# Performance work log

Measured on AMD Instinct MI355X. Metric: run time of the kernel, lower is better.

## Reference

```python
import jax, jax.numpy as jnp
import numpy as np

H = 32  # hidden_size hardcoded in CHIVE
T, B = 2048, 2048
D_F, D_P, D_S = 8, 8, 24


def setup_inputs() -> dict:
    key = jax.random.key(0)
    ks = jax.random.split(key, 16)
    s = 0.1  # weight scale
    return {
        "frnn_seq": jax.random.normal(ks[0], (T, B, D_F), jnp.float32),
        "phrnn_seq": jax.random.normal(ks[1], (T, B, D_P), jnp.float32),
        "sylrnn_seq": jax.random.normal(ks[2], (T, B, D_S), jnp.float32),
        "Wx_f": jax.random.normal(ks[3], (D_F, H), jnp.float32) * s,
        "Wh_f": jax.random.normal(ks[4], (H, H), jnp.float32) * s,
        "b_f": jnp.zeros((H,), jnp.float32),
        "Wx_p": jax.random.normal(ks[5], (D_P, H), jnp.float32) * s,
        "Wh_p": jax.random.normal(ks[6], (H, H), jnp.float32) * s,
        "b_p": jnp.zeros((H,), jnp.float32),
        "Wx_s": jax.random.normal(ks[7], (H, H), jnp.float32) * s,
        "Wh_s": jax.random.normal(ks[8], (H, H), jnp.float32) * s,
        "b_s": jnp.zeros((H,), jnp.float32),
        "frnn_clock": jax.random.randint(ks[9], (T,), 0, 8, jnp.int32),
        "phrnn_clock": jax.random.randint(ks[10], (T,), 0, 8, jnp.int32),
        "sample_freq": jax.random.randint(ks[11], (T,), 0, 2, jnp.int32),
    }


def reference(frnn_seq, phrnn_seq, sylrnn_seq,
              Wx_f, Wh_f, b_f, Wx_p, Wh_p, b_p, Wx_s, Wh_s, b_s,
              frnn_clock, phrnn_clock, sample_freq):
    # Clockwork cell: update h only when timestep % clock_val == 0.
    # Clocks are offset +1 so the modulus is always >= 1.
    t_idx = jnp.arange(T)
    upd_f = (t_idx % (frnn_clock + 1)) == 0          # [T] bool
    upd_p = (t_idx % (phrnn_clock + 1)) == 0
    # the syl layer updates exactly when sample_freq[t] == 1.
    upd_s = sample_freq == 1

    # Static pad of syl input to max_length = max(H, H, D_S) = H (D_S <= H).
    syl_padded = jnp.pad(sylrnn_seq, ((0, 0), (0, 0), (0, H - D_S)))  # [T,B,H]

    def cell(x, h, Wx, Wh, b, upd):
        h_new = jnp.tanh(x @ Wx + h @ Wh + b)
        return jnp.where(upd, h_new, h)

    def step(carry, inputs):
        h_f, h_p, h_s = carry
        x_f, x_p, x_s, uf, up, us = inputs
        h_f = cell(x_f, h_f, Wx_f, Wh_f, b_f, uf)        # [B,H]
        h_p = cell(x_p, h_p, Wx_p, Wh_p, b_p, up)        # [B,H]
        x_stack = jnp.stack([h_f, h_p, x_s], axis=0)     # [3,B,H]
        h_s = cell(x_stack, h_s, Wx_s, Wh_s, b_s, us)    # [3,B,H]
        return (h_f, h_p, h_s), None

    h0 = jnp.zeros((B, H), frnn_seq.dtype)
    h0s = jnp.zeros((3, B, H), frnn_seq.dtype)
    (h_f, h_p, h_s), _ = jax.lax.scan(
        step, (h0, h0, h0s),
        (frnn_seq, phrnn_seq, syl_padded, upd_f, upd_p, upd_s))
    return h_s
```

## Files before the change

kernel.cpp:

```cpp
#include <hip/hip_runtime.h>


constexpr int TS  = 2048;
constexpr int B   = 2048;
constexpr int HH  = 32;
constexpr int CH  = 16;
constexpr int NCH = TS / CH;
constexpr int BPB = 8;

__device__ __forceinline__ float fast_tanh(float x) {
    x = fminf(fmaxf(x, -9.0f), 9.0f);
    float e = __expf(2.0f * x);
    return (e - 1.0f) * __builtin_amdgcn_rcpf(e + 1.0f);
}

__global__ __launch_bounds__(256, 1)
void chive_rnn(const float* __restrict__ frnn, const float* __restrict__ phrnn,
               const float* __restrict__ syl,
               const float* __restrict__ Wxf, const float* __restrict__ Whf,
               const float* __restrict__ bf,
               const float* __restrict__ Wxp, const float* __restrict__ Whp,
               const float* __restrict__ bp,
               const float* __restrict__ Wxs, const float* __restrict__ Whs,
               const float* __restrict__ bs,
               const int* __restrict__ fclock, const int* __restrict__ pclock,
               const int* __restrict__ sfreq, float* __restrict__ out)
{
    __shared__ __align__(16) float xfb[2][CH][BPB * 8];
    __shared__ __align__(16) float xpb[2][CH][BPB * 8];
    __shared__ __align__(16) float xsb[2][CH][BPB * 24];
    __shared__ __align__(16) float hf[BPB][HH];
    __shared__ __align__(16) float hp[BPB][HH];
    __shared__ __align__(16) float hs[3][BPB][HH];
    __shared__ int gates[TS];

    const int tid = threadIdx.x;
    const int j   = tid & 31;
    const int g   = tid >> 5;
    const int b0  = blockIdx.x * BPB;

    float wxf[8], whf_r[32], wxp[8], whp_r[32], wxs_r[32], whs_r[32];
#pragma unroll
    for (int i = 0; i < 8;  i++) wxf[i]   = Wxf[i * HH + j];
#pragma unroll
    for (int i = 0; i < 32; i++) whf_r[i] = Whf[i * HH + j];
#pragma unroll
    for (int i = 0; i < 8;  i++) wxp[i]   = Wxp[i * HH + j];
#pragma unroll
    for (int i = 0; i < 32; i++) whp_r[i] = Whp[i * HH + j];
#pragma unroll
    for (int i = 0; i < 32; i++) wxs_r[i] = Wxs[i * HH + j];
#pragma unroll
    for (int i = 0; i < 32; i++) whs_r[i] = Whs[i * HH + j];
    const float bfj = bf[j], bpj = bp[j], bsj = bs[j];

    float4 rf, rp, rs0, rs1, rs2;
    const int tl = tid >> 4;
    const int q  = tid & 15;

    auto load_chunk = [&](int ch) {
        const size_t t  = (size_t)ch * CH + tl;
        const float* fb = frnn  + (t * B + b0) * 8;
        const float* pb = phrnn + (t * B + b0) * 8;
        const float* sb = syl   + (t * B + b0) * 24;
        rf  = *(const float4*)(fb + q * 4);
        rp  = *(const float4*)(pb + q * 4);
        rs0 = *(const float4*)(sb + q * 4);
        rs1 = *(const float4*)(sb + 64 + q * 4);
        rs2 = *(const float4*)(sb + 128 + q * 4);
    };
    auto store_chunk = [&](int buf) {
        *(float4*)&xfb[buf][tl][q * 4]       = rf;
        *(float4*)&xpb[buf][tl][q * 4]       = rp;
        *(float4*)&xsb[buf][tl][q * 4]       = rs0;
        *(float4*)&xsb[buf][tl][64 + q * 4]  = rs1;
        *(float4*)&xsb[buf][tl][128 + q * 4] = rs2;
    };

    load_chunk(0);

    for (int i = tid; i < TS; i += 256) {
        int mf = fclock[i] + 1;
        int mp = pclock[i] + 1;
        int v = 0;
        if ((i % mf) == 0)  v |= 1;
        if ((i % mp) == 0)  v |= 2;
        if (sfreq[i] == 1)  v |= 4;
        gates[i] = v;
    }

    hf[g][j] = 0.f; hp[g][j] = 0.f;
    hs[0][g][j] = 0.f; hs[1][g][j] = 0.f; hs[2][g][j] = 0.f;

    store_chunk(0);
    __syncthreads();

    int cur = 0;
#pragma unroll 1
    for (int ch = 0; ch < NCH; ch++) {
        if (ch + 1 < NCH) load_chunk(ch + 1);

#pragma unroll 1
        for (int c = 0; c < CH; c++) {
            const int t  = ch * CH + c;
            const int gt = __builtin_amdgcn_readfirstlane(gates[t]);

            if (gt & 1) {
                float4 a = {bfj, 0.f, 0.f, 0.f};
                const float4* xv = (const float4*)&xfb[cur][c][g * 8];
                float4 x0 = xv[0], x1 = xv[1];
                a.x = fmaf(x0.x, wxf[0], a.x); a.y = fmaf(x0.y, wxf[1], a.y);
                a.z = fmaf(x0.z, wxf[2], a.z); a.w = fmaf(x0.w, wxf[3], a.w);
                a.x = fmaf(x1.x, wxf[4], a.x); a.y = fmaf(x1.y, wxf[5], a.y);
                a.z = fmaf(x1.z, wxf[6], a.z); a.w = fmaf(x1.w, wxf[7], a.w);
#pragma unroll
                for (int kk = 0; kk < 8; kk++) {
                    float4 h4 = *(const float4*)&hf[g][kk * 4];
                    a.x = fmaf(h4.x, whf_r[kk*4+0], a.x);
                    a.y = fmaf(h4.y, whf_r[kk*4+1], a.y);
                    a.z = fmaf(h4.z, whf_r[kk*4+2], a.z);
                    a.w = fmaf(h4.w, whf_r[kk*4+3], a.w);
                }
                hf[g][j] = fast_tanh((a.x + a.y) + (a.z + a.w));
            }

            if (gt & 2) {
                float4 a = {bpj, 0.f, 0.f, 0.f};
                const float4* xv = (const float4*)&xpb[cur][c][g * 8];
                float4 x0 = xv[0], x1 = xv[1];
                a.x = fmaf(x0.x, wxp[0], a.x); a.y = fmaf(x0.y, wxp[1], a.y);
                a.z = fmaf(x0.z, wxp[2], a.z); a.w = fmaf(x0.w, wxp[3], a.w);
                a.x = fmaf(x1.x, wxp[4], a.x); a.y = fmaf(x1.y, wxp[5], a.y);
                a.z = fmaf(x1.z, wxp[6], a.z); a.w = fmaf(x1.w, wxp[7], a.w);
#pragma unroll
                for (int kk = 0; kk < 8; kk++) {
                    float4 h4 = *(const float4*)&hp[g][kk * 4];
                    a.x = fmaf(h4.x, whp_r[kk*4+0], a.x);
                    a.y = fmaf(h4.y, whp_r[kk*4+1], a.y);
                    a.z = fmaf(h4.z, whp_r[kk*4+2], a.z);
                    a.w = fmaf(h4.w, whp_r[kk*4+3], a.w);
                }
                hp[g][j] = fast_tanh((a.x + a.y) + (a.z + a.w));
            }

            if (gt & 4) {
                float4 a0 = {bsj, 0.f, 0.f, 0.f};
                float4 a1 = {bsj, 0.f, 0.f, 0.f};
                float4 a2 = {bsj, 0.f, 0.f, 0.f};
#pragma unroll
                for (int kk = 0; kk < 8; kk++) {
                    float4 hf4 = *(const float4*)&hf[g][kk * 4];
                    float4 hp4 = *(const float4*)&hp[g][kk * 4];
                    float w0 = wxs_r[kk*4+0], w1 = wxs_r[kk*4+1];
                    float w2 = wxs_r[kk*4+2], w3 = wxs_r[kk*4+3];
                    a0.x = fmaf(hf4.x, w0, a0.x); a0.y = fmaf(hf4.y, w1, a0.y);
                    a0.z = fmaf(hf4.z, w2, a0.z); a0.w = fmaf(hf4.w, w3, a0.w);
                    a1.x = fmaf(hp4.x, w0, a1.x); a1.y = fmaf(hp4.y, w1, a1.y);
                    a1.z = fmaf(hp4.z, w2, a1.z); a1.w = fmaf(hp4.w, w3, a1.w);
                }
#pragma unroll
                for (int kk = 0; kk < 6; kk++) {
                    float4 x4 = *(const float4*)&xsb[cur][c][g * 24 + kk * 4];
                    a2.x = fmaf(x4.x, wxs_r[kk*4+0], a2.x);
                    a2.y = fmaf(x4.y, wxs_r[kk*4+1], a2.y);
                    a2.z = fmaf(x4.z, wxs_r[kk*4+2], a2.z);
                    a2.w = fmaf(x4.w, wxs_r[kk*4+3], a2.w);
                }
#pragma unroll
                for (int kk = 0; kk < 8; kk++) {
                    float4 h0 = *(const float4*)&hs[0][g][kk * 4];
                    float4 h1 = *(const float4*)&hs[1][g][kk * 4];
                    float4 h2 = *(const float4*)&hs[2][g][kk * 4];
                    float w0 = whs_r[kk*4+0], w1 = whs_r[kk*4+1];
                    float w2 = whs_r[kk*4+2], w3 = whs_r[kk*4+3];
                    a0.x = fmaf(h0.x, w0, a0.x); a0.y = fmaf(h0.y, w1, a0.y);
                    a0.z = fmaf(h0.z, w2, a0.z); a0.w = fmaf(h0.w, w3, a0.w);
                    a1.x = fmaf(h1.x, w0, a1.x); a1.y = fmaf(h1.y, w1, a1.y);
                    a1.z = fmaf(h1.z, w2, a1.z); a1.w = fmaf(h1.w, w3, a1.w);
                    a2.x = fmaf(h2.x, w0, a2.x); a2.y = fmaf(h2.y, w1, a2.y);
                    a2.z = fmaf(h2.z, w2, a2.z); a2.w = fmaf(h2.w, w3, a2.w);
                }
                hs[0][g][j] = fast_tanh((a0.x + a0.y) + (a0.z + a0.w));
                hs[1][g][j] = fast_tanh((a1.x + a1.y) + (a1.z + a1.w));
                hs[2][g][j] = fast_tanh((a2.x + a2.y) + (a2.z + a2.w));
            }
        }

        if (ch + 1 < NCH) store_chunk(cur ^ 1);
        __syncthreads();
        cur ^= 1;
    }

    const int b = b0 + g;
    out[((size_t)0 * B + b) * HH + j] = hs[0][g][j];
    out[((size_t)1 * B + b) * HH + j] = hs[1][g][j];
    out[((size_t)2 * B + b) * HH + j] = hs[2][g][j];
}

extern "C" void kernel_launch(void* const* d_in, const int* in_sizes, int n_in,
                              void* d_out, int out_size, void* d_ws, size_t ws_size,
                              hipStream_t stream) {
    const float* frnn  = (const float*)d_in[0];
    const float* phrnn = (const float*)d_in[1];
    const float* syl   = (const float*)d_in[2];
    const float* Wxf   = (const float*)d_in[3];
    const float* Whf   = (const float*)d_in[4];
    const float* bf    = (const float*)d_in[5];
    const float* Wxp   = (const float*)d_in[6];
    const float* Whp   = (const float*)d_in[7];
    const float* bp    = (const float*)d_in[8];
    const float* Wxs   = (const float*)d_in[9];
    const float* Whs   = (const float*)d_in[10];
    const float* bs    = (const float*)d_in[11];
    const int* fclock  = (const int*)d_in[12];
    const int* pclock  = (const int*)d_in[13];
    const int* sfreq   = (const int*)d_in[14];
    float* out = (float*)d_out;

    dim3 grid(B / BPB);
    dim3 block(256);
    chive_rnn<<<grid, block, 0, stream>>>(frnn, phrnn, syl,
                                          Wxf, Whf, bf, Wxp, Whp, bp,
                                          Wxs, Whs, bs,
                                          fclock, pclock, sfreq, out);
}
```

Before: 1.664 ms.

## Keep recurrent hidden states in registers and exchange via DPP/swizzle

Hidden states move from LDS arrays into per-lane registers. Each 32-wide matvec is now done with ds_swizzle and DPP lane permutations, using weights preloaded in an XOR-permuted order so that each lane's rotating operand meets the matching weight. The syl input is repacked into a 32-wide zero-padded LDS layout so each lane can read its own element. This removes the LDS round trips and the implicit dependencies on every recurrent step. In exchange it adds many cross-lane permute instructions, and ds_swizzle still goes through the LDS hardware.

```diff
diff --git a/kernel.cpp b/kernel.cpp
--- a/kernel.cpp
+++ b/kernel.cpp
@@ -8,10 +8,58 @@
 constexpr int NCH = TS / CH;
 constexpr int BPB = 8;
 
+#define XD1(x) __int_as_float(__builtin_amdgcn_mov_dpp(__float_as_int(x), 0xB1, 0xF, 0xF, true))
+#define XD2(x) __int_as_float(__builtin_amdgcn_mov_dpp(__float_as_int(x), 0x4E, 0xF, 0xF, true))
+#define SWZ(x, imm) __int_as_float(__builtin_amdgcn_ds_swizzle(__float_as_int(x), imm))
+
 __device__ __forceinline__ float fast_tanh(float x) {
     x = fminf(fmaxf(x, -9.0f), 9.0f);
     float e = __expf(2.0f * x);
     return (e - 1.0f) * __builtin_amdgcn_rcpf(e + 1.0f);
+}
+
+__device__ __forceinline__ float dot32(float v, const float* wt) {
+    float r0 = v;
+    float r1 = SWZ(v, 0x201F);
+    float r2 = SWZ(v, 0x401F);
+    float r3 = SWZ(v, 0x601F);
+    float a0 = r0 * wt[0], a1 = r1 * wt[8], a2 = r2 * wt[16], a3 = r3 * wt[24];
+    r0 = XD1(r0); r1 = XD1(r1); r2 = XD1(r2); r3 = XD1(r3);
+    a0 = fmaf(r0, wt[1], a0); a1 = fmaf(r1, wt[9],  a1);
+    a2 = fmaf(r2, wt[17], a2); a3 = fmaf(r3, wt[25], a3);
+    r0 = XD2(r0); r1 = XD2(r1); r2 = XD2(r2); r3 = XD2(r3);
+    a0 = fmaf(r0, wt[2], a0); a1 = fmaf(r1, wt[10], a1);
+    a2 = fmaf(r2, wt[18], a2); a3 = fmaf(r3, wt[26], a3);
+    r0 = XD1(r0); r1 = XD1(r1); r2 = XD1(r2); r3 = XD1(r3);
+    a0 = fmaf(r0, wt[3], a0); a1 = fmaf(r1, wt[11], a1);
+    a2 = fmaf(r2, wt[19], a2); a3 = fmaf(r3, wt[27], a3);
+    r0 = SWZ(r0, 0x101F); r1 = SWZ(r1, 0x101F);
+    r2 = SWZ(r2, 0x101F); r3 = SWZ(r3, 0x101F);
+    a0 = fmaf(r0, wt[4], a0); a1 = fmaf(r1, wt[12], a1);
+    a2 = fmaf(r2, wt[20], a2); a3 = fmaf(r3, wt[28], a3);
+    r0 = XD1(r0); r1 = XD1(r1); r2 = XD1(r2); r3 = XD1(r3);
+    a0 = fmaf(r0, wt[5], a0); a1 = fmaf(r1, wt[13], a1);
+    a2 = fmaf(r2, wt[21], a2); a3 = fmaf(r3, wt[29], a3);
+    r0 = XD2(r0); r1 = XD2(r1); r2 = XD2(r2); r3 = XD2(r3);
+    a0 = fmaf(r0, wt[6], a0); a1 = fmaf(r1, wt[14], a1);
+    a2 = fmaf(r2, wt[22], a2); a3 = fmaf(r3, wt[30], a3);
+    r0 = XD1(r0); r1 = XD1(r1); r2 = XD1(r2); r3 = XD1(r3);
+    a0 = fmaf(r0, wt[7], a0); a1 = fmaf(r1, wt[15], a1);
+    a2 = fmaf(r2, wt[23], a2); a3 = fmaf(r3, wt[31], a3);
+    return (a0 + a1) + (a2 + a3);
+}
+
+__device__ __forceinline__ float dot8(float v, const float* wt) {
+    float r0 = v;
+    float r1 = SWZ(v, 0x101F);
+    float a0 = r0 * wt[0], a1 = r1 * wt[4];
+    r0 = XD1(r0); r1 = XD1(r1);
+    a0 = fmaf(r0, wt[1], a0); a1 = fmaf(r1, wt[5], a1);
+    r0 = XD2(r0); r1 = XD2(r1);
+    a0 = fmaf(r0, wt[2], a0); a1 = fmaf(r1, wt[6], a1);
+    r0 = XD1(r0); r1 = XD1(r1);
+    a0 = fmaf(r0, wt[3], a0); a1 = fmaf(r1, wt[7], a1);
+    return a0 + a1;
 }
 
 __global__ __launch_bounds__(256, 1)
@@ -28,10 +76,7 @@
 {
     __shared__ __align__(16) float xfb[2][CH][BPB * 8];
     __shared__ __align__(16) float xpb[2][CH][BPB * 8];
-    __shared__ __align__(16) float xsb[2][CH][BPB * 24];
-    __shared__ __align__(16) float hf[BPB][HH];
-    __shared__ __align__(16) float hp[BPB][HH];
-    __shared__ __align__(16) float hs[3][BPB][HH];
+    __shared__ __align__(16) float xsb[2][CH][BPB * 32];
     __shared__ int gates[TS];
 
     const int tid = threadIdx.x;
@@ -39,25 +84,52 @@
     const int g   = tid >> 5;
     const int b0  = blockIdx.x * BPB;
 
-    float wxf[8], whf_r[32], wxp[8], whp_r[32], wxs_r[32], whs_r[32];
-#pragma unroll
-    for (int i = 0; i < 8;  i++) wxf[i]   = Wxf[i * HH + j];
-#pragma unroll
-    for (int i = 0; i < 32; i++) whf_r[i] = Whf[i * HH + j];
-#pragma unroll
-    for (int i = 0; i < 8;  i++) wxp[i]   = Wxp[i * HH + j];
-#pragma unroll
-    for (int i = 0; i < 32; i++) whp_r[i] = Whp[i * HH + j];
-#pragma unroll
-    for (int i = 0; i < 32; i++) wxs_r[i] = Wxs[i * HH + j];
-#pragma unroll
-    for (int i = 0; i < 32; i++) whs_r[i] = Whs[i * HH + j];
+    const int g3v[8] = {0, 1, 3, 2, 6, 7, 5, 4};
+    const int g2v[4] = {0, 1, 3, 2};
+    float whf_t[32], whp_t[32], wxs_t[32], whs_t[32], wxf_t[8], wxp_t[8];
+#pragma unroll
+    for (int c = 0; c < 4; c++) {
+#pragma unroll
+        for (int i = 0; i < 8; i++) {
+            const int k = j ^ ((c << 3) | g3v[i]);
+            whf_t[c * 8 + i] = Whf[k * HH + j];
+            whp_t[c * 8 + i] = Whp[k * HH + j];
+            wxs_t[c * 8 + i] = Wxs[k * HH + j];
+            whs_t[c * 8 + i] = Whs[k * HH + j];
+        }
+    }
+#pragma unroll
+    for (int c = 0; c < 2; c++) {
+#pragma unroll
+        for (int i = 0; i < 4; i++) {
+            const int k = (j & 7) ^ ((c << 2) | g2v[i]);
+            wxf_t[c * 4 + i] = Wxf[k * HH + j];
+            wxp_t[c * 4 + i] = Wxp[k * HH + j];
+        }
+    }
     const float bfj = bf[j], bpj = bp[j], bsj = bs[j];
 
-    float4 rf, rp, rs0, rs1, rs2;
+#pragma unroll
+    for (int i = 0; i < 32; i++) {
+        asm volatile("" : "+v"(whf_t[i]), "+v"(whp_t[i]), "+v"(wxs_t[i]), "+v"(whs_t[i]));
+    }
+#pragma unroll
+    for (int i = 0; i < 8; i++) {
+        asm volatile("" : "+v"(wxf_t[i]), "+v"(wxp_t[i]));
+    }
+
     const int tl = tid >> 4;
     const int q  = tid & 15;
-
+    int sb_[3], ss_[3];
+#pragma unroll
+    for (int u = 0; u < 3; u++) {
+        const int r = q + 16 * u;
+        sb_[u] = r / 6;
+        ss_[u] = r - 6 * sb_[u];
+    }
+    const int zslot = ((q >> 1) * 8 + 6 + (q & 1)) * 4;
+
+    float4 rf, rp, rsA, rsB, rsC;
     auto load_chunk = [&](int ch) {
         const size_t t  = (size_t)ch * CH + tl;
         const float* fb = frnn  + (t * B + b0) * 8;
@@ -65,35 +137,36 @@
         const float* sb = syl   + (t * B + b0) * 24;
         rf  = *(const float4*)(fb + q * 4);
         rp  = *(const float4*)(pb + q * 4);
-        rs0 = *(const float4*)(sb + q * 4);
-        rs1 = *(const float4*)(sb + 64 + q * 4);
-        rs2 = *(const float4*)(sb + 128 + q * 4);
+        rsA = *(const float4*)(sb + (q +  0) * 4);
+        rsB = *(const float4*)(sb + (q + 16) * 4);
+        rsC = *(const float4*)(sb + (q + 32) * 4);
     };
     auto store_chunk = [&](int buf) {
-        *(float4*)&xfb[buf][tl][q * 4]       = rf;
-        *(float4*)&xpb[buf][tl][q * 4]       = rp;
-        *(float4*)&xsb[buf][tl][q * 4]       = rs0;
-        *(float4*)&xsb[buf][tl][64 + q * 4]  = rs1;
-        *(float4*)&xsb[buf][tl][128 + q * 4] = rs2;
+        *(float4*)&xfb[buf][tl][q * 4] = rf;
+        *(float4*)&xpb[buf][tl][q * 4] = rp;
+        *(float4*)&xsb[buf][tl][(sb_[0] * 8 + ss_[0]) * 4] = rsA;
+        *(float4*)&xsb[buf][tl][(sb_[1] * 8 + ss_[1]) * 4] = rsB;
+        *(float4*)&xsb[buf][tl][(sb_[2] * 8 + ss_[2]) * 4] = rsC;
+        const float4 z4 = {0.f, 0.f, 0.f, 0.f};
+        *(float4*)&xsb[buf][tl][zslot] = z4;
     };
 
     load_chunk(0);
 
     for (int i = tid; i < TS; i += 256) {
-        int mf = fclock[i] + 1;
-        int mp = pclock[i] + 1;
+        const int mf = fclock[i] + 1;
+        const int mp = pclock[i] + 1;
         int v = 0;
-        if ((i % mf) == 0)  v |= 1;
-        if ((i % mp) == 0)  v |= 2;
-        if (sfreq[i] == 1)  v |= 4;
+        if ((i % mf) == 0) v |= 1;
+        if ((i % mp) == 0) v |= 2;
+        if (sfreq[i] == 1) v |= 4;
         gates[i] = v;
     }
-
-    hf[g][j] = 0.f; hp[g][j] = 0.f;
-    hs[0][g][j] = 0.f; hs[1][g][j] = 0.f; hs[2][g][j] = 0.f;
 
     store_chunk(0);
     __syncthreads();
+
+    float vhf = 0.f, vhp = 0.f, vhs0 = 0.f, vhs1 = 0.f, vhs2 = 0.f;
 
     int cur = 0;
 #pragma unroll 1
@@ -106,83 +179,21 @@
             const int gt = __builtin_amdgcn_readfirstlane(gates[t]);
 
             if (gt & 1) {
-                float4 a = {bfj, 0.f, 0.f, 0.f};
-                const float4* xv = (const float4*)&xfb[cur][c][g * 8];
-                float4 x0 = xv[0], x1 = xv[1];
-                a.x = fmaf(x0.x, wxf[0], a.x); a.y = fmaf(x0.y, wxf[1], a.y);
-                a.z = fmaf(x0.z, wxf[2], a.z); a.w = fmaf(x0.w, wxf[3], a.w);
-                a.x = fmaf(x1.x, wxf[4], a.x); a.y = fmaf(x1.y, wxf[5], a.y);
-                a.z = fmaf(x1.z, wxf[6], a.z); a.w = fmaf(x1.w, wxf[7], a.w);
-#pragma unroll
-                for (int kk = 0; kk < 8; kk++) {
-                    float4 h4 = *(const float4*)&hf[g][kk * 4];
-                    a.x = fmaf(h4.x, whf_r[kk*4+0], a.x);
-                    a.y = fmaf(h4.y, whf_r[kk*4+1], a.y);
-                    a.z = fmaf(h4.z, whf_r[kk*4+2], a.z);
-                    a.w = fmaf(h4.w, whf_r[kk*4+3], a.w);
-                }
-                hf[g][j] = fast_tanh((a.x + a.y) + (a.z + a.w));
+                const float xf = xfb[cur][c][g * 8 + (j & 7)];
+                vhf = fast_tanh(bfj + dot8(xf, wxf_t) + dot32(vhf, whf_t));
             }
-
             if (gt & 2) {
-                float4 a = {bpj, 0.f, 0.f, 0.f};
-                const float4* xv = (const float4*)&xpb[cur][c][g * 8];
-                float4 x0 = xv[0], x1 = xv[1];
-                a.x = fmaf(x0.x, wxp[0], a.x); a.y = fmaf(x0.y, wxp[1], a.y);
-                a.z = fmaf(x0.z, wxp[2], a.z); a.w = fmaf(x0.w, wxp[3], a.w);
-                a.x = fmaf(x1.x, wxp[4], a.x); a.y = fmaf(x1.y, wxp[5], a.y);
-                a.z = fmaf(x1.z, wxp[6], a.z); a.w = fmaf(x1.w, wxp[7], a.w);
-#pragma unroll
-                for (int kk = 0; kk < 8; kk++) {
-                    float4 h4 = *(const float4*)&hp[g][kk * 4];
-                    a.x = fmaf(h4.x, whp_r[kk*4+0], a.x);
-                    a.y = fmaf(h4.y, whp_r[kk*4+1], a.y);
-                    a.z = fmaf(h4.z, whp_r[kk*4+2], a.z);
-                    a.w = fmaf(h4.w, whp_r[kk*4+3], a.w);
-                }
-                hp[g][j] = fast_tanh((a.x + a.y) + (a.z + a.w));
+                const float xp = xpb[cur][c][g * 8 + (j & 7)];
+                vhp = fast_tanh(bpj + dot8(xp, wxp_t) + dot32(vhp, whp_t));
             }
-
             if (gt & 4) {
-                float4 a0 = {bsj, 0.f, 0.f, 0.f};
-                float4 a1 = {bsj, 0.f, 0.f, 0.f};
-                float4 a2 = {bsj, 0.f, 0.f, 0.f};
-#pragma unroll
-                for (int kk = 0; kk < 8; kk++) {
-                    float4 hf4 = *(const float4*)&hf[g][kk * 4];
-                    float4 hp4 = *(const float4*)&hp[g][kk * 4];
-                    float w0 = wxs_r[kk*4+0], w1 = wxs_r[kk*4+1];
-                    float w2 = wxs_r[kk*4+2], w3 = wxs_r[kk*4+3];
-                    a0.x = fmaf(hf4.x, w0, a0.x); a0.y = fmaf(hf4.y, w1, a0.y);
-                    a0.z = fmaf(hf4.z, w2, a0.z); a0.w = fmaf(hf4.w, w3, a0.w);
-                    a1.x = fmaf(hp4.x, w0, a1.x); a1.y = fmaf(hp4.y, w1, a1.y);
-                    a1.z = fmaf(hp4.z, w2, a1.z); a1.w = fmaf(hp4.w, w3, a1.w);
-                }
-#pragma unroll
-                for (int kk = 0; kk < 6; kk++) {
-                    float4 x4 = *(const float4*)&xsb[cur][c][g * 24 + kk * 4];
-                    a2.x = fmaf(x4.x, wxs_r[kk*4+0], a2.x);
-                    a2.y = fmaf(x4.y, wxs_r[kk*4+1], a2.y);
-                    a2.z = fmaf(x4.z, wxs_r[kk*4+2], a2.z);
-                    a2.w = fmaf(x4.w, wxs_r[kk*4+3], a2.w);
-                }
-#pragma unroll
-                for (int kk = 0; kk < 8; kk++) {
-                    float4 h0 = *(const float4*)&hs[0][g][kk * 4];
-                    float4 h1 = *(const float4*)&hs[1][g][kk * 4];
-                    float4 h2 = *(const float4*)&hs[2][g][kk * 4];
-                    float w0 = whs_r[kk*4+0], w1 = whs_r[kk*4+1];
-                    float w2 = whs_r[kk*4+2], w3 = whs_r[kk*4+3];
-                    a0.x = fmaf(h0.x, w0, a0.x); a0.y = fmaf(h0.y, w1, a0.y);
-                    a0.z = fmaf(h0.z, w2, a0.z); a0.w = fmaf(h0.w, w3, a0.w);
-                    a1.x = fmaf(h1.x, w0, a1.x); a1.y = fmaf(h1.y, w1, a1.y);
-                    a1.z = fmaf(h1.z, w2, a1.z); a1.w = fmaf(h1.w, w3, a1.w);
-                    a2.x = fmaf(h2.x, w0, a2.x); a2.y = fmaf(h2.y, w1, a2.y);
-                    a2.z = fmaf(h2.z, w2, a2.z); a2.w = fmaf(h2.w, w3, a2.w);
-                }
-                hs[0][g][j] = fast_tanh((a0.x + a0.y) + (a0.z + a0.w));
-                hs[1][g][j] = fast_tanh((a1.x + a1.y) + (a1.z + a1.w));
-                hs[2][g][j] = fast_tanh((a2.x + a2.y) + (a2.z + a2.w));
+                const float xs = xsb[cur][c][g * 32 + j];
+                const float p0 = bsj + dot32(vhf, wxs_t) + dot32(vhs0, whs_t);
+                const float p1 = bsj + dot32(vhp, wxs_t) + dot32(vhs1, whs_t);
+                const float p2 = bsj + dot32(xs,  wxs_t) + dot32(vhs2, whs_t);
+                vhs0 = fast_tanh(p0);
+                vhs1 = fast_tanh(p1);
+                vhs2 = fast_tanh(p2);
             }
         }
 
@@ -192,9 +203,9 @@
     }
 
     const int b = b0 + g;
-    out[((size_t)0 * B + b) * HH + j] = hs[0][g][j];
-    out[((size_t)1 * B + b) * HH + j] = hs[1][g][j];
-    out[((size_t)2 * B + b) * HH + j] = hs[2][g][j];
+    out[((size_t)0 * B + b) * HH + j] = vhs0;
+    out[((size_t)1 * B + b) * HH + j] = vhs1;
+    out[((size_t)2 * B + b) * HH + j] = vhs2;
 }
 
 extern "C" void kernel_launch(void* const* d_in, const int* in_sizes, int n_in,
```

Result: slower. 1.759 ms (+5.7%).
